# Kernel tuning notes

Measured on AMD Instinct MI355X. Metric: run time of the kernel, lower is better.

## Reference

```python
import jax, jax.numpy as jnp
import numpy as np

N_X, N_U, N_Y = 256, 32, 32
BATCH, T = 16, 8192
LAM_MIN, LAM_MAX = 0.9, 0.995
B_SCALE, D_SCALE = 0.25, 0.25


def setup_inputs() -> dict:
    key = jax.random.key(0)
    k = jax.random.split(key, 6)
    # Orthogonal Q via QR of a random Gaussian matrix (as in the torch module)
    M = jax.random.normal(k[0], (N_X, N_X), dtype=jnp.float32)
    Q, _ = jnp.linalg.qr(M)
    lam = LAM_MIN + (LAM_MAX - LAM_MIN) * jax.random.uniform(k[1], (N_X,), dtype=jnp.float32)
    Bmat = B_SCALE * jax.random.normal(k[2], (N_X, N_U), dtype=jnp.float32)
    # C picks out the first n_y coordinates (C[i, i] = 1)
    C = jnp.eye(N_Y, N_X, dtype=jnp.float32)
    D = D_SCALE * jax.random.normal(k[3], (N_Y, N_U), dtype=jnp.float32)
    x0 = jax.random.normal(k[4], (BATCH, N_X), dtype=jnp.float32)
    u = jax.random.normal(k[5], (BATCH, T, N_U), dtype=jnp.float32)
    return {"x0": x0, "u": u, "Q": Q, "lam": lam, "Bmat": Bmat, "C": C, "D": D}


def _diag_scan(lam, v):
    """Diagonal linear recurrence x_t = lam * x_{t-1} + v_t (x_0 folded into v[:, 0]).

    lam: (N,), v: (B, T, N) -> states x_1..x_T of shape (B, T, N).
    """
    a = jnp.broadcast_to(lam, v.shape)

    def op(l, r):
        a1, b1 = l
        a2, b2 = r
        return a1 * a2, a2 * b1 + b2

    return jax.lax.associative_scan(op, (a, v), axis=1)[1]


def reference(x0, u, Q, lam, Bmat, C, D):
    Bz = Q.T @ Bmat            # (n_x, n_u) modal input matrix
    Cz = C @ Q                 # (n_y, n_x) modal output matrix
    z0 = x0 @ Q                # (B, n_x)   modal initial state
    v = jnp.einsum('btu,nu->btn', u, Bz)   # (B, T, n_x)
    v = v.at[:, 0].add(lam * z0)            # fold lam * z0 into first step
    z_next = _diag_scan(lam, v)             # (B, T, n_x) = z_1..z_T
    # y_t uses z_t for t = 0..T-1 (states[:, :-1] in the original)
    z_prev = jnp.concatenate([z0[:, None, :], z_next[:, :-1]], axis=1)
    y = jnp.einsum('btn,yn->bty', z_prev, Cz) + jnp.einsum('btu,yu->bty', u, D)
    return y
```

## Files before the change

### kernel.cpp

```cpp
#include <hip/hip_runtime.h>

typedef _Float16 half4_t __attribute__((ext_vector_type(4)));
typedef _Float16 half8_t __attribute__((ext_vector_type(8)));
typedef float f32x4 __attribute__((ext_vector_type(4)));

constexpr int NX = 256, NU = 32, NY = 32, BATCH = 16, T = 8192;
constexpr int NC = 64, L = 128;
constexpr int SUBT = 32, NSUB = L / SUBT;
constexpr int KW = NX + NU;
constexpr int ZP = 264;

__global__ __launch_bounds__(256) void k_pre(
    const float* __restrict__ x0, const float* __restrict__ Q,
    const float* __restrict__ Bm, const float* __restrict__ C,
    const float* __restrict__ D,
    _Float16* __restrict__ Bzh, _Float16* __restrict__ Wh, float* __restrict__ z0)
{
    int o = blockIdx.x * 64 + (threadIdx.x >> 2);
    int p = threadIdx.x & 3;
    if (o >= 20480) {
        if (p == 0) {
            int g = o - 20480, iy = g >> 5, j = g & 31;
            Wh[iy * KW + NX + j] = (_Float16)D[iy * NU + j];
        }
        return;
    }
    float s = 0.f;
    int k0 = p * 64;
    if (o < 8192) {
        int n = o >> 5, j = o & 31;
        for (int k = k0; k < k0 + 64; ++k) s = fmaf(Q[k * NX + n], Bm[k * NU + j], s);
    } else if (o < 16384) {
        int g = o - 8192; int iy = g >> 8, nn = g & 255;
        for (int k = k0; k < k0 + 64; ++k) s = fmaf(C[iy * NX + k], Q[k * NX + nn], s);
    } else {
        int g = o - 16384; int b = g >> 8, nn = g & 255;
        for (int k = k0; k < k0 + 64; ++k) s = fmaf(x0[b * NX + k], Q[k * NX + nn], s);
    }
    s += __shfl_xor(s, 1);
    s += __shfl_xor(s, 2);
    if (p == 0) {
        if (o < 8192) {
            Bzh[o] = (_Float16)s;
        } else if (o < 16384) {
            int g = o - 8192; int iy = g >> 8, nn = g & 255;
            Wh[iy * KW + nn] = (_Float16)s;
        } else {
            z0[o - 16384] = s;
        }
    }
}

__global__ __launch_bounds__(256) void k_phase1(
    const float* __restrict__ u, const float* __restrict__ lam,
    const _Float16* __restrict__ Bzh, float* __restrict__ S)
{
    __shared__ __align__(16) _Float16 ut[2][SUBT][32];

    const int b = blockIdx.x >> 6, c = blockIdx.x & 63, tid = threadIdx.x;
    const int w = tid >> 6, lane = tid & 63, m16 = lane & 15, quad = lane >> 4;

    half8_t bfrag[4];
    #pragma unroll
    for (int i = 0; i < 4; ++i)
        bfrag[i] = *(const half8_t*)&Bzh[((4 * w + i) * 16 + m16) * NU + quad * 8];

    float wr[4][4], wt16[4], l32[4], acc[4];
    #pragma unroll
    for (int i = 0; i < 4; ++i) {
        float la = lam[(4 * w + i) * 16 + m16];
        float p2 = la * la, p4 = p2 * p2, p8 = p4 * p4, p16 = p8 * p8;
        float inv1 = 1.0f / la;
        float inv4 = (inv1 * inv1) * (inv1 * inv1);
        float pq = 1.0f;
        if (quad & 1) pq *= inv4;
        if (quad & 2) pq *= inv4 * inv4;
        float w0 = (p16 * p8 * p4 * p2 * la) * pq;
        wr[i][0] = w0;
        wr[i][1] = w0 * inv1;
        wr[i][2] = wr[i][1] * inv1;
        wr[i][3] = wr[i][2] * inv1;
        wt16[i] = 1.0f / p16;
        l32[i] = p16 * p16;
        acc[i] = 0.f;
    }

    const float* ug = u + ((size_t)(b * T) + (size_t)c * L) * NU;

    for (int sub = 0; sub < NSUB; ++sub) {
        {
            float4 uu = *(const float4*)(ug + (size_t)sub * SUBT * NU + tid * 4);
            int tr = tid >> 3, cb = ((tid & 7) * 4 + (tr & 3) * 8) & 31;
            half4_t h; h.x = (_Float16)uu.x; h.y = (_Float16)uu.y;
            h.z = (_Float16)uu.z; h.w = (_Float16)uu.w;
            *(half4_t*)&ut[sub & 1][tr][cb] = h;
        }
        __syncthreads();
        int rot = (m16 & 3) * 8;
        half8_t af0 = *(const half8_t*)&ut[sub & 1][m16][(quad * 8 + rot) & 31];
        half8_t af1 = *(const half8_t*)&ut[sub & 1][16 + m16][(quad * 8 + rot) & 31];
        #pragma unroll
        for (int i = 0; i < 4; ++i) {
            f32x4 z4 = {0.f, 0.f, 0.f, 0.f};
            f32x4 v0 = __builtin_amdgcn_mfma_f32_16x16x32_f16(af0, bfrag[i], z4, 0, 0, 0);
            f32x4 v1 = __builtin_amdgcn_mfma_f32_16x16x32_f16(af1, bfrag[i], z4, 0, 0, 0);
            float s0 = wr[i][0] * v0[0] + wr[i][1] * v0[1] + wr[i][2] * v0[2] + wr[i][3] * v0[3];
            float s1 = wr[i][0] * v1[0] + wr[i][1] * v1[1] + wr[i][2] * v1[2] + wr[i][3] * v1[3];
            acc[i] = fmaf(l32[i], acc[i], fmaf(wt16[i], s1, s0));
        }
    }
    #pragma unroll
    for (int i = 0; i < 4; ++i) {
        acc[i] += __shfl_xor(acc[i], 16);
        acc[i] += __shfl_xor(acc[i], 32);
    }
    float out = quad == 0 ? acc[0] : quad == 1 ? acc[1] : quad == 2 ? acc[2] : acc[3];
    S[(size_t)blockIdx.x * NX + (4 * w + quad) * 16 + m16] = out;
}

__global__ __launch_bounds__(256) void k_phase3(
    const float* __restrict__ u, const float* __restrict__ lam,
    const _Float16* __restrict__ Bzh, const _Float16* __restrict__ Wh,
    const float* __restrict__ S, const float* __restrict__ z0,
    float* __restrict__ y)
{
    __shared__ __align__(16) _Float16 ut[2][SUBT][32];
    __shared__ __align__(16) _Float16 zt[SUBT][ZP];
    __shared__ float pvec[NX];

    const int b = blockIdx.x >> 6, c = blockIdx.x & 63, tid = threadIdx.x;
    const int w = tid >> 6, lane = tid & 63, m16 = lane & 15, quad = lane >> 4;
    const int tw = w & 1, yw = w >> 1;

    {
        float la = lam[tid];
        float l2L = 128.0f * __log2f(la);
        const float* Sb = S + (size_t)(b * NC) * NX + tid;
        float pv = 0.f;
        #pragma unroll 8
        for (int k = 0; k < c; ++k) {
            float wgt = exp2f((float)k * l2L);
            pv = fmaf(wgt, Sb[(size_t)(c - 1 - k) * NX], pv);
        }
        pvec[tid] = fmaf(exp2f((float)c * l2L), z0[b * NX + tid], pv);
    }

    half8_t bfrag[4];
    #pragma unroll
    for (int i = 0; i < 4; ++i)
        bfrag[i] = *(const half8_t*)&Bzh[((4 * w + i) * 16 + m16) * NU + quad * 8];
    half8_t wfrag[9];
    #pragma unroll
    for (int kk = 0; kk < 9; ++kk)
        wfrag[kk] = *(const half8_t*)&Wh[(yw * 16 + m16) * KW + kk * 32 + quad * 8];

    float lamn[4], inv1[4], iq[4], i16p[4], fq[4], f16p[4], l32[4], p[4];
    #pragma unroll
    for (int i = 0; i < 4; ++i) {
        int ni = (4 * w + i) * 16 + m16;
        float la = lam[ni];
        lamn[i] = la;
        float p2 = la * la, p4 = p2 * p2, p8 = p4 * p4, p16 = p8 * p8;
        float iv = 1.0f / la;
        inv1[i] = iv;
        float iv4 = (iv * iv) * (iv * iv);
        float pqi = 1.0f, pqf = 1.0f;
        if (quad & 1) { pqi *= iv4; pqf *= p4; }
        if (quad & 2) { pqi *= iv4 * iv4; pqf *= p8; }
        iq[i] = iv * pqi;
        fq[i] = pqf;
        i16p[i] = 1.0f / p16;
        f16p[i] = p16;
        l32[i] = p16 * p16;
    }
    __syncthreads();
    #pragma unroll
    for (int i = 0; i < 4; ++i)
        p[i] = pvec[(4 * w + i) * 16 + m16];

    const float* ug = u + ((size_t)(b * T) + (size_t)c * L) * NU;
    float* yg = y + ((size_t)(b * T) + (size_t)c * L) * NY;
    const int rot = (m16 & 3) * 8;

    for (int sub = 0; sub < NSUB; ++sub) {
        {
            float4 uu = *(const float4*)(ug + (size_t)sub * SUBT * NU + tid * 4);
            int tr = tid >> 3, cb = ((tid & 7) * 4 + (tr & 3) * 8) & 31;
            half4_t h; h.x = (_Float16)uu.x; h.y = (_Float16)uu.y;
            h.z = (_Float16)uu.z; h.w = (_Float16)uu.w;
            *(half4_t*)&ut[sub & 1][tr][cb] = h;
        }
        __syncthreads();

        half8_t af0 = *(const half8_t*)&ut[sub & 1][m16][(quad * 8 + rot) & 31];
        half8_t af1 = *(const half8_t*)&ut[sub & 1][16 + m16][(quad * 8 + rot) & 31];
        #pragma unroll
        for (int i = 0; i < 4; ++i) {
            int ni = (4 * w + i) * 16 + m16;
            f32x4 z4 = {0.f, 0.f, 0.f, 0.f};
            f32x4 v0 = __builtin_amdgcn_mfma_f32_16x16x32_f16(af0, bfrag[i], z4, 0, 0, 0);
            f32x4 v1 = __builtin_amdgcn_mfma_f32_16x16x32_f16(af1, bfrag[i], z4, 0, 0, 0);
            float a0[4], a1[4];
            float sc = iq[i];
            #pragma unroll
            for (int r = 0; r < 4; ++r) {
                a0[r] = v0[r] * sc;
                a1[r] = v1[r] * (sc * i16p[i]);
                sc *= inv1[i];
            }
            float e0[4], e1[4];
            e0[0] = 0.f; e0[1] = a0[0]; e0[2] = e0[1] + a0[1]; e0[3] = e0[2] + a0[2];
            float S40 = e0[3] + a0[3];
            e1[0] = 0.f; e1[1] = a1[0]; e1[2] = e1[1] + a1[1]; e1[3] = e1[2] + a1[2];
            float S41 = e1[3] + a1[3];
            float incl0 = S40;
            float t0 = __shfl_up(incl0, 16); if (quad >= 1) incl0 += t0;
            t0 = __shfl_up(incl0, 32);       if (quad >= 2) incl0 += t0;
            float excl0 = incl0 - S40;
            float total0 = __shfl(incl0, 48 + m16);
            float incl1 = S41;
            float t1 = __shfl_up(incl1, 16); if (quad >= 1) incl1 += t1;
            t1 = __shfl_up(incl1, 32);       if (quad >= 2) incl1 += t1;
            float excl1 = incl1 - S41;
            float total1 = __shfl(incl1, 48 + m16);
            float f = fq[i];
            #pragma unroll
            for (int r = 0; r < 4; ++r) {
                float zv0 = f * (p[i] + (excl0 + e0[r]));
                float zv1 = (f * f16p[i]) * (p[i] + (total0 + excl1 + e1[r]));
                zt[quad * 4 + r][ni] = (_Float16)zv0;
                zt[16 + quad * 4 + r][ni] = (_Float16)zv1;
                f *= lamn[i];
            }
            p[i] = l32[i] * (p[i] + (total0 + total1));
        }
        __syncthreads();

        f32x4 acc = {0.f, 0.f, 0.f, 0.f};
        #pragma unroll
        for (int kk = 0; kk < 8; ++kk) {
            half8_t az = *(const half8_t*)&zt[tw * 16 + m16][kk * 32 + quad * 8];
            acc = __builtin_amdgcn_mfma_f32_16x16x32_f16(az, wfrag[kk], acc, 0, 0, 0);
        }
        {
            half8_t au = *(const half8_t*)&ut[sub & 1][tw * 16 + m16][(quad * 8 + rot) & 31];
            acc = __builtin_amdgcn_mfma_f32_16x16x32_f16(au, wfrag[8], acc, 0, 0, 0);
        }
        #pragma unroll
        for (int r = 0; r < 4; ++r)
            yg[(size_t)(sub * SUBT + tw * 16 + quad * 4 + r) * NY + yw * 16 + m16] = acc[r];
    }
}

extern "C" void kernel_launch(void* const* d_in, const int* in_sizes, int n_in,
                              void* d_out, int out_size, void* d_ws, size_t ws_size,
                              hipStream_t stream) {
    (void)in_sizes; (void)n_in; (void)out_size; (void)ws_size;
    const float* x0  = (const float*)d_in[0];
    const float* u   = (const float*)d_in[1];
    const float* Q   = (const float*)d_in[2];
    const float* lam = (const float*)d_in[3];
    const float* Bm  = (const float*)d_in[4];
    const float* C   = (const float*)d_in[5];
    const float* D   = (const float*)d_in[6];
    float* y = (float*)d_out;

    char* ws = (char*)d_ws;
    _Float16* Bzh = (_Float16*)(ws);
    _Float16* Wh  = (_Float16*)(ws + 16384);
    float*    z0  = (float*)(ws + 34816);
    float*    S   = (float*)(ws + 51200);

    k_pre   <<<336, 256, 0, stream>>>(x0, Q, Bm, C, D, Bzh, Wh, z0);
    k_phase1<<<BATCH * NC, 256, 0, stream>>>(u, lam, Bzh, S);
    k_phase3<<<BATCH * NC, 256, 0, stream>>>(u, lam, Bzh, Wh, S, z0, y);
}
```

Baseline: 118.6 us.

## Halve chunk length, double chunks, and prefetch whole u chunk up front

Shrinks the per-block chunk from 128 to 64 timesteps, which doubles the number of chunks and blocks so the GPU gets more parallelism. Both phase kernels now load the whole u chunk into registers at kernel start and stage it into shared memory once, instead of doing a load and barrier per sub-step. This is meant to hide global load latency. It also adds occupancy hints to the launch bounds. The cost is that phase 3's serial prefix loop over previous chunk sums gets longer (up to 127 iterations) and the S buffer doubles in size.

```diff
diff --git a/kernel.cpp b/kernel.cpp
--- a/kernel.cpp
+++ b/kernel.cpp
@@ -5,7 +5,7 @@
 typedef float f32x4 __attribute__((ext_vector_type(4)));
 
 constexpr int NX = 256, NU = 32, NY = 32, BATCH = 16, T = 8192;
-constexpr int NC = 64, L = 128;
+constexpr int NC = 128, L = 64;
 constexpr int SUBT = 32, NSUB = L / SUBT;
 constexpr int KW = NX + NU;
 constexpr int ZP = 264;
@@ -51,54 +51,63 @@
     }
 }
 
-__global__ __launch_bounds__(256) void k_phase1(
+__global__ __launch_bounds__(256, 4) void k_phase1(
     const float* __restrict__ u, const float* __restrict__ lam,
     const _Float16* __restrict__ Bzh, float* __restrict__ S)
 {
-    __shared__ __align__(16) _Float16 ut[2][SUBT][32];
-
-    const int b = blockIdx.x >> 6, c = blockIdx.x & 63, tid = threadIdx.x;
+    __shared__ __align__(16) _Float16 ut[NSUB][SUBT][32];
+
+    const int b = blockIdx.x >> 7, c = blockIdx.x & 127, tid = threadIdx.x;
     const int w = tid >> 6, lane = tid & 63, m16 = lane & 15, quad = lane >> 4;
+    const int rot = (m16 & 3) * 8;
+
+    const float* ug = u + ((size_t)(b * T) + (size_t)c * L) * NU;
+
+    float4 uu[NSUB];
+    #pragma unroll
+    for (int s = 0; s < NSUB; ++s)
+        uu[s] = *(const float4*)(ug + (size_t)s * SUBT * NU + tid * 4);
 
     half8_t bfrag[4];
     #pragma unroll
     for (int i = 0; i < 4; ++i)
         bfrag[i] = *(const half8_t*)&Bzh[((4 * w + i) * 16 + m16) * NU + quad * 8];
+
+    {
+        int tr = tid >> 3, cb = ((tid & 7) * 4 + (tr & 3) * 8) & 31;
+        #pragma unroll
+        for (int s = 0; s < NSUB; ++s) {
+            half4_t h; h.x = (_Float16)uu[s].x; h.y = (_Float16)uu[s].y;
+            h.z = (_Float16)uu[s].z; h.w = (_Float16)uu[s].w;
+            *(half4_t*)&ut[s][tr][cb] = h;
+        }
+    }
 
     float wr[4][4], wt16[4], l32[4], acc[4];
     #pragma unroll
     for (int i = 0; i < 4; ++i) {
         float la = lam[(4 * w + i) * 16 + m16];
         float p2 = la * la, p4 = p2 * p2, p8 = p4 * p4, p16 = p8 * p8;
-        float inv1 = 1.0f / la;
-        float inv4 = (inv1 * inv1) * (inv1 * inv1);
+        float iv = 1.0f / la;
+        float iv4 = (iv * iv) * (iv * iv);
         float pq = 1.0f;
-        if (quad & 1) pq *= inv4;
-        if (quad & 2) pq *= inv4 * inv4;
+        if (quad & 1) pq *= iv4;
+        if (quad & 2) pq *= iv4 * iv4;
         float w0 = (p16 * p8 * p4 * p2 * la) * pq;
         wr[i][0] = w0;
-        wr[i][1] = w0 * inv1;
-        wr[i][2] = wr[i][1] * inv1;
-        wr[i][3] = wr[i][2] * inv1;
+        wr[i][1] = w0 * iv;
+        wr[i][2] = wr[i][1] * iv;
+        wr[i][3] = wr[i][2] * iv;
         wt16[i] = 1.0f / p16;
         l32[i] = p16 * p16;
         acc[i] = 0.f;
     }
-
-    const float* ug = u + ((size_t)(b * T) + (size_t)c * L) * NU;
-
+    __syncthreads();
+
+    #pragma unroll
     for (int sub = 0; sub < NSUB; ++sub) {
-        {
-            float4 uu = *(const float4*)(ug + (size_t)sub * SUBT * NU + tid * 4);
-            int tr = tid >> 3, cb = ((tid & 7) * 4 + (tr & 3) * 8) & 31;
-            half4_t h; h.x = (_Float16)uu.x; h.y = (_Float16)uu.y;
-            h.z = (_Float16)uu.z; h.w = (_Float16)uu.w;
-            *(half4_t*)&ut[sub & 1][tr][cb] = h;
-        }
-        __syncthreads();
-        int rot = (m16 & 3) * 8;
-        half8_t af0 = *(const half8_t*)&ut[sub & 1][m16][(quad * 8 + rot) & 31];
-        half8_t af1 = *(const half8_t*)&ut[sub & 1][16 + m16][(quad * 8 + rot) & 31];
+        half8_t af0 = *(const half8_t*)&ut[sub][m16][(quad * 8 + rot) & 31];
+        half8_t af1 = *(const half8_t*)&ut[sub][16 + m16][(quad * 8 + rot) & 31];
         #pragma unroll
         for (int i = 0; i < 4; ++i) {
             f32x4 z4 = {0.f, 0.f, 0.f, 0.f};
@@ -118,23 +127,31 @@
     S[(size_t)blockIdx.x * NX + (4 * w + quad) * 16 + m16] = out;
 }
 
-__global__ __launch_bounds__(256) void k_phase3(
+__global__ __launch_bounds__(256, 4) void k_phase3(
     const float* __restrict__ u, const float* __restrict__ lam,
     const _Float16* __restrict__ Bzh, const _Float16* __restrict__ Wh,
     const float* __restrict__ S, const float* __restrict__ z0,
     float* __restrict__ y)
 {
-    __shared__ __align__(16) _Float16 ut[2][SUBT][32];
+    __shared__ __align__(16) _Float16 ut[NSUB][SUBT][32];
     __shared__ __align__(16) _Float16 zt[SUBT][ZP];
     __shared__ float pvec[NX];
 
-    const int b = blockIdx.x >> 6, c = blockIdx.x & 63, tid = threadIdx.x;
+    const int b = blockIdx.x >> 7, c = blockIdx.x & 127, tid = threadIdx.x;
     const int w = tid >> 6, lane = tid & 63, m16 = lane & 15, quad = lane >> 4;
     const int tw = w & 1, yw = w >> 1;
+    const int rot = (m16 & 3) * 8;
+
+    const float* ug = u + ((size_t)(b * T) + (size_t)c * L) * NU;
+
+    float4 uu[NSUB];
+    #pragma unroll
+    for (int s = 0; s < NSUB; ++s)
+        uu[s] = *(const float4*)(ug + (size_t)s * SUBT * NU + tid * 4);
 
     {
         float la = lam[tid];
-        float l2L = 128.0f * __log2f(la);
+        float l2L = 64.0f * __log2f(la);
         const float* Sb = S + (size_t)(b * NC) * NX + tid;
         float pv = 0.f;
         #pragma unroll 8
@@ -143,6 +160,16 @@
             pv = fmaf(wgt, Sb[(size_t)(c - 1 - k) * NX], pv);
         }
         pvec[tid] = fmaf(exp2f((float)c * l2L), z0[b * NX + tid], pv);
+    }
+
+    {
+        int tr = tid >> 3, cb = ((tid & 7) * 4 + (tr & 3) * 8) & 31;
+        #pragma unroll
+        for (int s = 0; s < NSUB; ++s) {
+            half4_t h; h.x = (_Float16)uu[s].x; h.y = (_Float16)uu[s].y;
+            h.z = (_Float16)uu[s].z; h.w = (_Float16)uu[s].w;
+            *(half4_t*)&ut[s][tr][cb] = h;
+        }
     }
 
     half8_t bfrag[4];
@@ -178,22 +205,12 @@
     for (int i = 0; i < 4; ++i)
         p[i] = pvec[(4 * w + i) * 16 + m16];
 
-    const float* ug = u + ((size_t)(b * T) + (size_t)c * L) * NU;
     float* yg = y + ((size_t)(b * T) + (size_t)c * L) * NY;
-    const int rot = (m16 & 3) * 8;
-
+
+    #pragma unroll
     for (int sub = 0; sub < NSUB; ++sub) {
-        {
-            float4 uu = *(const float4*)(ug + (size_t)sub * SUBT * NU + tid * 4);
-            int tr = tid >> 3, cb = ((tid & 7) * 4 + (tr & 3) * 8) & 31;
-            half4_t h; h.x = (_Float16)uu.x; h.y = (_Float16)uu.y;
-            h.z = (_Float16)uu.z; h.w = (_Float16)uu.w;
-            *(half4_t*)&ut[sub & 1][tr][cb] = h;
-        }
-        __syncthreads();
-
-        half8_t af0 = *(const half8_t*)&ut[sub & 1][m16][(quad * 8 + rot) & 31];
-        half8_t af1 = *(const half8_t*)&ut[sub & 1][16 + m16][(quad * 8 + rot) & 31];
+        half8_t af0 = *(const half8_t*)&ut[sub][m16][(quad * 8 + rot) & 31];
+        half8_t af1 = *(const half8_t*)&ut[sub][16 + m16][(quad * 8 + rot) & 31];
         #pragma unroll
         for (int i = 0; i < 4; ++i) {
             int ni = (4 * w + i) * 16 + m16;
@@ -243,12 +260,13 @@
             acc = __builtin_amdgcn_mfma_f32_16x16x32_f16(az, wfrag[kk], acc, 0, 0, 0);
         }
         {
-            half8_t au = *(const half8_t*)&ut[sub & 1][tw * 16 + m16][(quad * 8 + rot) & 31];
+            half8_t au = *(const half8_t*)&ut[sub][tw * 16 + m16][(quad * 8 + rot) & 31];
             acc = __builtin_amdgcn_mfma_f32_16x16x32_f16(au, wfrag[8], acc, 0, 0, 0);
         }
         #pragma unroll
         for (int r = 0; r < 4; ++r)
             yg[(size_t)(sub * SUBT + tw * 16 + quad * 4 + r) * NY + yw * 16 + m16] = acc[r];
+        __syncthreads();
     }
 }
 
```

After: 145.0 us. 1.22x slower.
